# Optimization experiments

Hardware: AMD Instinct MI355X
Metric: run time of the kernel (lower is better)

Reference implementation:

```python
import jax, jax.numpy as jnp
import numpy as np


def setup_inputs() -> dict:
    key = jax.random.key(0)
    ks = jax.random.split(key, 5)
    B, N, C = 64, 384, 768
    return {
        "x": jax.random.normal(ks[0], (B, N, C), dtype=jnp.float32),
        "x_hsi": jax.random.normal(ks[1], (B, N, C), dtype=jnp.float32),
        "qkv_w": jax.random.normal(ks[2], (3 * C, C), dtype=jnp.float32) * 0.02,
        "proj_w": jax.random.normal(ks[3], (C, C), dtype=jnp.float32) * 0.02,
        "proj_b": jax.random.normal(ks[4], (C,), dtype=jnp.float32) * 0.02,
        "t_h": 8,
        "t_w": 8,
        "s_h": 16,
        "s_w": 16,
        "num_heads": 12,
    }


def reference(x, x_hsi, qkv_w, proj_w, proj_b, t_h, t_w, s_h, s_w, num_heads):
    B, N, C = x.shape
    H = num_heads
    Dh = C // H
    scale = Dh ** -0.5
    Lt = t_h * t_w * 2  # template tokens (2 templates)

    def qkv_heads(inp):
        qkv = (inp @ qkv_w.T).reshape(B, N, 3, H, Dh)
        qkv = jnp.transpose(qkv, (2, 0, 3, 1, 4))  # [3,B,H,N,Dh]
        return qkv[0], qkv[1], qkv[2]

    q, k, v = qkv_heads(x)
    q_hsi, k_hsi, v_hsi = qkv_heads(x_hsi)

    q_mt, q_s = q[:, :, :Lt], q[:, :, Lt:]
    k_mt, v_mt = k[:, :, :Lt], v[:, :, :Lt]
    q_s_hsi = q_hsi[:, :, Lt:]

    def attn(qq, kk, vv):
        a = jax.nn.softmax(jnp.einsum('bhqd,bhkd->bhqk', qq, kk) * scale, axis=-1)
        o = jnp.einsum('bhqk,bhkd->bhqd', a, vv)
        return jnp.transpose(o, (0, 2, 1, 3)).reshape(B, -1, C)

    x_mt = attn(q_mt, k_mt, v_mt)        # template-template
    x_s = attn(q_s, k, v)                # search attends to all
    x_s_hsi = attn(q_s_hsi, k_hsi, v_hsi)  # hsi search attends to all hsi

    out = jnp.concatenate([x_mt, x_s], axis=1) @ proj_w.T + proj_b
    out_hsi = jnp.concatenate([x_mt, x_s_hsi], axis=1) @ proj_w.T + proj_b
    return out, out_hsi
```

## Files before the change

kernel.cpp:

```cpp
#include <hip/hip_runtime.h>

typedef __attribute__((ext_vector_type(8))) short short8;
typedef __attribute__((ext_vector_type(4))) short bf16x4;
typedef __attribute__((ext_vector_type(4))) float f32x4;

__device__ __forceinline__ f32x4 mfma16(short8 a, short8 b, f32x4 c) {
  return __builtin_amdgcn_mfma_f32_16x16x32_bf16(a, b, c, 0, 0, 0);
}

__device__ __forceinline__ short f2bf(float f) {
  union { float f; unsigned u; } v; v.f = f;
  unsigned r = (v.u + 0x7fffu + ((v.u >> 16) & 1u)) >> 16;
  return (short)r;
}

__device__ __forceinline__ void gload16(const short* g, short* l) {
  __builtin_amdgcn_global_load_lds(
      (const __attribute__((address_space(1))) void*)g,
      (__attribute__((address_space(3))) void*)l, 16, 0, 0);
}

__global__ __launch_bounds__(256) void cvt_k(const float* __restrict__ src,
                                             short* __restrict__ dst, long n8) {
  long i = (long)blockIdx.x * 256 + threadIdx.x;
  const long stride = (long)gridDim.x * 256;
  for (; i < n8; i += stride) {
    float4 a = *(const float4*)(src + i * 8);
    float4 b = *(const float4*)(src + i * 8 + 4);
    short8 o = {f2bf(a.x), f2bf(a.y), f2bf(a.z), f2bf(a.w),
                f2bf(b.x), f2bf(b.y), f2bf(b.z), f2bf(b.w)};
    *(short8*)(dst + i * 8) = o;
  }
}

__device__ __forceinline__ void gemm256_core(
    const short* a00, const short* a01, const short* a10, const short* a11,
    const short* b00, const short* b01, const short* b10, const short* b11,
    char* lds, int wv, int lane, f32x4 (&acc)[8][4]) {
  const int l15 = lane & 15, q4 = lane >> 4;
  const int wm = wv & 1, wn = wv >> 1;
  const char* rdA = lds + wm * 16384;
  const char* rdB = lds + 32768 + (wn >> 1) * 16384;
  const int rB0 = (wn & 1) * 64;

  auto stg = [&](int T, int h, int tt) {
    const int t = tt >= 12 ? tt - 12 : tt;
    char* d = lds + (t & 1) * 65536 + T * 32768 + h * 16384 + wv * 2048;
    const short* g0 = T ? (h ? b10 : b00) : (h ? a10 : a00);
    const short* g1 = T ? (h ? b11 : b01) : (h ? a11 : a01);
    gload16(g0 + t * 64, (short*)d);
    gload16(g1 + t * 64, (short*)(d + 1024));
  };
  auto rdfrag = [&](const char* base, int rowl, int ks) -> short8 {
    int off = ks * 8192 + rowl * 64 + q4 * 16;
    off ^= ((off >> 9) & 1) << 5;
    return *(const short8*)(base + off);
  };

  stg(0, 0, 0); stg(0, 1, 0); stg(1, 0, 0); stg(1, 1, 0);
  stg(1, 0, 1); stg(1, 1, 1);
  asm volatile("s_waitcnt vmcnt(4)" ::: "memory");
  __builtin_amdgcn_s_barrier();

  auto ktile = [&](int buf, int t) {
    const char* A = rdA + buf * 65536;
    const char* B = rdB + buf * 65536;
    short8 af[4][2], bfr[4][2];
#pragma unroll
    for (int m = 0; m < 4; ++m) {
      af[m][0] = rdfrag(A, m * 16 + l15, 0);
      af[m][1] = rdfrag(A, m * 16 + l15, 1);
    }
#pragma unroll
    for (int n = 0; n < 2; ++n) {
      bfr[n][0] = rdfrag(B, rB0 + n * 16 + l15, 0);
      bfr[n][1] = rdfrag(B, rB0 + n * 16 + l15, 1);
    }
    stg(0, 0, t + 1);
    __builtin_amdgcn_s_barrier();
    __builtin_amdgcn_s_setprio(1);
#pragma unroll
    for (int m = 0; m < 4; ++m)
#pragma unroll
      for (int n = 0; n < 2; ++n) {
        acc[m][n] = mfma16(af[m][0], bfr[n][0], acc[m][n]);
        acc[m][n] = mfma16(af[m][1], bfr[n][1], acc[m][n]);
      }
    __builtin_amdgcn_s_setprio(0);
    __builtin_amdgcn_s_barrier();
#pragma unroll
    for (int n = 2; n < 4; ++n) {
      bfr[n][0] = rdfrag(B, rB0 + n * 16 + l15, 0);
      bfr[n][1] = rdfrag(B, rB0 + n * 16 + l15, 1);
    }
    stg(0, 1, t + 1);
    __builtin_amdgcn_s_barrier();
    __builtin_amdgcn_s_setprio(1);
#pragma unroll
    for (int m = 0; m < 4; ++m)
#pragma unroll
      for (int n = 2; n < 4; ++n) {
        acc[m][n] = mfma16(af[m][0], bfr[n][0], acc[m][n]);
        acc[m][n] = mfma16(af[m][1], bfr[n][1], acc[m][n]);
      }
    __builtin_amdgcn_s_setprio(0);
    __builtin_amdgcn_s_barrier();
#pragma unroll
    for (int m = 0; m < 4; ++m) {
      af[m][0] = rdfrag(A, (m + 4) * 16 + l15, 0);
      af[m][1] = rdfrag(A, (m + 4) * 16 + l15, 1);
    }
    stg(1, 0, t + 2);
    __builtin_amdgcn_s_barrier();
    __builtin_amdgcn_s_setprio(1);
#pragma unroll
    for (int m = 0; m < 4; ++m)
#pragma unroll
      for (int n = 0; n < 2; ++n) {
        acc[m + 4][n] = mfma16(af[m][0], bfr[n][0], acc[m + 4][n]);
        acc[m + 4][n] = mfma16(af[m][1], bfr[n][1], acc[m + 4][n]);
      }
    __builtin_amdgcn_s_setprio(0);
    __builtin_amdgcn_s_barrier();
    stg(1, 1, t + 2);
    __builtin_amdgcn_s_barrier();
    __builtin_amdgcn_s_setprio(1);
#pragma unroll
    for (int m = 0; m < 4; ++m)
#pragma unroll
      for (int n = 2; n < 4; ++n) {
        acc[m + 4][n] = mfma16(af[m][0], bfr[n][0], acc[m + 4][n]);
        acc[m + 4][n] = mfma16(af[m][1], bfr[n][1], acc[m + 4][n]);
      }
    __builtin_amdgcn_s_setprio(0);
    asm volatile("s_waitcnt vmcnt(4)" ::: "memory");
    __builtin_amdgcn_s_barrier();
  };

  for (int g = 0; g < 6; ++g) {
    ktile(0, 2 * g);
    ktile(1, 2 * g + 1);
  }
}

__device__ __forceinline__ void stage_geom(int wv, int lane, int* srow, int* coff) {
#pragma unroll
  for (int j = 0; j < 2; ++j) {
    const int s = wv * 128 + j * 64 + lane;
    srow[j] = (s >> 2) & 127;
    coff[j] = (s >> 9) * 32 + (((((s & 3) << 4) ^ (((s >> 5) & 1) << 5))) >> 1);
  }
}

__global__ __launch_bounds__(512, 2) void gemm_qkv_k(
    const short* __restrict__ A0, const short* __restrict__ A1,
    const short* __restrict__ W,
    short* __restrict__ O0, short* __restrict__ O1) {
  extern __shared__ char lds[];
  const int tid = threadIdx.x, lane = tid & 63, wv = tid >> 6;
  const int l15 = lane & 15, q4 = lane >> 4;
  const int m0 = blockIdx.x * 256, n0 = blockIdx.y * 256;
  const short* A = blockIdx.z ? A1 : A0;
  short* O = blockIdx.z ? O1 : O0;

  int srow[2], coff[2];
  stage_geom(wv, lane, srow, coff);
  const short* a00 = A + (long)(m0 + srow[0]) * 768 + coff[0];
  const short* a01 = A + (long)(m0 + srow[1]) * 768 + coff[1];
  const short* a10 = A + (long)(m0 + 128 + srow[0]) * 768 + coff[0];
  const short* a11 = A + (long)(m0 + 128 + srow[1]) * 768 + coff[1];
  const short* b00 = W + (long)(n0 + srow[0]) * 768 + coff[0];
  const short* b01 = W + (long)(n0 + srow[1]) * 768 + coff[1];
  const short* b10 = W + (long)(n0 + 128 + srow[0]) * 768 + coff[0];
  const short* b11 = W + (long)(n0 + 128 + srow[1]) * 768 + coff[1];

  f32x4 acc[8][4] = {};
  gemm256_core(a00, a01, a10, a11, b00, b01, b10, b11, lds, wv, lane, acc);

  const int wm = wv & 1, wn = wv >> 1;
#pragma unroll
  for (int m = 0; m < 8; ++m)
#pragma unroll
    for (int n = 0; n < 4; ++n) {
      const int col = n0 + wn * 64 + n * 16 + l15;
#pragma unroll
      for (int r = 0; r < 4; ++r) {
        const int row = m0 + wm * 128 + m * 16 + q4 * 4 + r;
        O[(long)row * 2304 + col] = f2bf(acc[m][n][r]);
      }
    }
}

template <int NK>
__global__ __launch_bounds__(256) void attn_k(
    const short* __restrict__ qkvx, const short* __restrict__ qkvh,
    short* __restrict__ omt, short* __restrict__ os, short* __restrict__ osh) {
  constexpr int NT = NK / 16;
  constexpr int KT = NK / 64;
  constexpr int T = (NK == 128) ? 2 : 8;
  __shared__ __align__(16) short kv[2][64 * 72];
  __shared__ __align__(16) short sp[2][4][16 * 72];

  const int tid = threadIdx.x, lane = tid & 63, wv = tid >> 6;
  const int l15 = lane & 15, q4 = lane >> 4;
  const int bx = blockIdx.x;
  const int b = bx / (12 * T);
  const int rr = bx % (12 * T);
  const int h = rr / T, t = rr % T;

  const short* src;
  short* outb;
  int q0;
  if (NK == 128) {
    src = qkvx;
    outb = omt + ((long)b * 128 + t * 64) * 768 + h * 64;
    q0 = t * 64;
  } else {
    const int tt = t & 3;
    const bool hs = t >= 4;
    src = hs ? qkvh : qkvx;
    outb = (hs ? osh : os) + ((long)b * 256 + tt * 64) * 768 + h * 64;
    q0 = 128 + tt * 64;
  }
  const short* qb = src + ((long)(b * 384 + q0 + wv * 16)) * 2304 + h * 64;
  const short* kb = src + (long)b * 384 * 2304 + 768 + h * 64;
  const short* vb = kb + 768;

  const int key0 = tid >> 3, dg0 = tid & 7;
  const int key1 = key0 + 32, dg1 = dg0;

  short8 qf0 = *(const short8*)(qb + (long)l15 * 2304 + q4 * 8);
  short8 qf1 = *(const short8*)(qb + (long)l15 * 2304 + 32 + q4 * 8);

  f32x4 sacc[NT] = {};
  short8 ka0 = *(const short8*)(kb + (long)key0 * 2304 + dg0 * 8);
  short8 ka1 = *(const short8*)(kb + (long)key1 * 2304 + dg1 * 8);
#pragma unroll
  for (int kt = 0; kt < KT; ++kt) {
    const int buf = kt & 1;
    *(short8*)&kv[buf][key0 * 72 + dg0 * 8] = ka0;
    *(short8*)&kv[buf][key1 * 72 + dg1 * 8] = ka1;
    __syncthreads();
    if (kt + 1 < KT) {
      ka0 = *(const short8*)(kb + (long)((kt + 1) * 64 + key0) * 2304 + dg0 * 8);
      ka1 = *(const short8*)(kb + (long)((kt + 1) * 64 + key1) * 2304 + dg1 * 8);
    }
#pragma unroll
    for (int j = 0; j < 4; ++j) {
      short8 kf0 = *(const short8*)&kv[buf][(j * 16 + l15) * 72 + q4 * 8];
      short8 kf1 = *(const short8*)&kv[buf][(j * 16 + l15) * 72 + 32 + q4 * 8];
      sacc[kt * 4 + j] = mfma16(qf0, kf0, sacc[kt * 4 + j]);
      sacc[kt * 4 + j] = mfma16(qf1, kf1, sacc[kt * 4 + j]);
    }
  }

  short8 va0 = *(const short8*)(vb + (long)key0 * 2304 + dg0 * 8);
  short8 va1 = *(const short8*)(vb + (long)key1 * 2304 + dg1 * 8);

  const float scale = 0.125f;
  float mx[4] = {-3e38f, -3e38f, -3e38f, -3e38f};
#pragma unroll
  for (int nt = 0; nt < NT; ++nt)
#pragma unroll
    for (int r = 0; r < 4; ++r) mx[r] = fmaxf(mx[r], sacc[nt][r]);
#pragma unroll
  for (int r = 0; r < 4; ++r) {
    mx[r] = fmaxf(mx[r], __shfl_xor(mx[r], 1));
    mx[r] = fmaxf(mx[r], __shfl_xor(mx[r], 2));
    mx[r] = fmaxf(mx[r], __shfl_xor(mx[r], 4));
    mx[r] = fmaxf(mx[r], __shfl_xor(mx[r], 8));
  }
  float sm[4] = {0.f, 0.f, 0.f, 0.f};
  unsigned pb[NT][2];
#pragma unroll
  for (int nt = 0; nt < NT; ++nt) {
    float ev[4];
#pragma unroll
    for (int r = 0; r < 4; ++r) {
      ev[r] = __expf((sacc[nt][r] - mx[r]) * scale);
      sm[r] += ev[r];
    }
    pb[nt][0] = (unsigned)(unsigned short)f2bf(ev[0]) |
                ((unsigned)(unsigned short)f2bf(ev[1]) << 16);
    pb[nt][1] = (unsigned)(unsigned short)f2bf(ev[2]) |
                ((unsigned)(unsigned short)f2bf(ev[3]) << 16);
  }
#pragma unroll
  for (int r = 0; r < 4; ++r) {
    sm[r] += __shfl_xor(sm[r], 1);
    sm[r] += __shfl_xor(sm[r], 2);
    sm[r] += __shfl_xor(sm[r], 4);
    sm[r] += __shfl_xor(sm[r], 8);
  }

  f32x4 oacc[4] = {};
#pragma unroll
  for (int kt = 0; kt < KT; ++kt) {
    const int buf = kt & 1;
    char* vt = (char*)&kv[buf][0];
#pragma unroll
    for (int e = 0; e < 8; ++e) {
      const int d0 = dg0 * 8 + e;
      *(short*)(vt + ((d0 * 144 + key0 * 2) ^ (dg0 << 4))) = va0[e];
      *(short*)(vt + ((d0 * 144 + key1 * 2) ^ (dg1 << 4))) = va1[e];
    }
    short* spw = &sp[buf][wv][0];
#pragma unroll
    for (int nt2 = 0; nt2 < 4; ++nt2) {
#pragma unroll
      for (int p = 0; p < 2; ++p) {
        const unsigned w = pb[kt * 4 + nt2][p];
        spw[(q4 * 4 + 2 * p) * 72 + nt2 * 16 + l15] = (short)(w & 0xffffu);
        spw[(q4 * 4 + 2 * p + 1) * 72 + nt2 * 16 + l15] = (short)(w >> 16);
      }
    }
    __syncthreads();
    if (kt + 1 < KT) {
      va0 = *(const short8*)(vb + (long)((kt + 1) * 64 + key0) * 2304 + dg0 * 8);
      va1 = *(const short8*)(vb + (long)((kt + 1) * 64 + key1) * 2304 + dg1 * 8);
    }
#pragma unroll
    for (int ks = 0; ks < 2; ++ks) {
      short8 pf = *(const short8*)&sp[buf][wv][l15 * 72 + ks * 32 + q4 * 8];
#pragma unroll
      for (int n2 = 0; n2 < 4; ++n2) {
        const int db = n2 * 16 + l15;
        short8 vf = *(const short8*)(vt + ((db * 144 + (ks * 32 + q4 * 8) * 2) ^
                                           (((db >> 3) & 7) << 4)));
        oacc[n2] = mfma16(pf, vf, oacc[n2]);
      }
    }
  }

  short* ob = outb + wv * 16 * 768;
#pragma unroll
  for (int r = 0; r < 4; ++r) {
    const float inv = 1.f / sm[r];
#pragma unroll
    for (int n2 = 0; n2 < 4; ++n2)
      ob[(q4 * 4 + r) * 768 + n2 * 16 + l15] = f2bf(oacc[n2][r] * inv);
  }
}

__global__ __launch_bounds__(512, 2) void gemm_proj_k(
    const short* __restrict__ mt, const short* __restrict__ sA,
    const short* __restrict__ sh,
    const short* __restrict__ W, const float* __restrict__ bias,
    float* __restrict__ out, int cb0) {
  extern __shared__ char lds[];
  const int tid = threadIdx.x, lane = tid & 63, wv = tid >> 6;
  const int l15 = lane & 15, q4 = lane >> 4;
  const int m0 = blockIdx.x * 256, n0 = blockIdx.y * 256;
  const short* s = blockIdx.z ? sh : sA;

  int srow[2], coff[2];
  stage_geom(wv, lane, srow, coff);
  auto arow = [&](int r) -> const short* {
    const int ba = r / 384, na = r % 384;
    return na < 128 ? (mt + ((long)ba * 128 + na) * 768)
                    : (s + ((long)ba * 256 + (na - 128)) * 768);
  };
  const short* a00 = arow(m0 + srow[0]) + coff[0];
  const short* a01 = arow(m0 + srow[1]) + coff[1];
  const short* a10 = arow(m0 + 128 + srow[0]) + coff[0];
  const short* a11 = arow(m0 + 128 + srow[1]) + coff[1];
  const short* b00 = W + (long)(n0 + srow[0]) * 768 + coff[0];
  const short* b01 = W + (long)(n0 + srow[1]) * 768 + coff[1];
  const short* b10 = W + (long)(n0 + 128 + srow[0]) * 768 + coff[0];
  const short* b11 = W + (long)(n0 + 128 + srow[1]) * 768 + coff[1];

  f32x4 acc[8][4] = {};
  gemm256_core(a00, a01, a10, a11, b00, b01, b10, b11, lds, wv, lane, acc);

  const int wm = wv & 1, wn = wv >> 1;
#pragma unroll
  for (int n = 0; n < 4; ++n) {
    const int col = n0 + wn * 64 + n * 16 + l15;
    const float bvv = bias[col];
#pragma unroll
    for (int m = 0; m < 8; ++m)
#pragma unroll
      for (int r = 0; r < 4; ++r) {
        const int row = m0 + wm * 128 + m * 16 + q4 * 4 + r;
        out[(long)blockIdx.z * 18874368 + ((long)cb0 * 384 + row) * 768 + col] =
            acc[m][n][r] + bvv;
      }
  }
}

extern "C" void kernel_launch(void* const* d_in, const int* in_sizes, int n_in,
                              void* d_out, int out_size, void* d_ws, size_t ws_size,
                              hipStream_t stream) {
  (void)in_sizes; (void)n_in; (void)out_size;
  const float* x  = (const float*)d_in[0];
  const float* xh = (const float*)d_in[1];
  const float* qw = (const float*)d_in[2];
  const float* pw = (const float*)d_in[3];
  const float* pb = (const float*)d_in[4];
  float* out = (float*)d_out;

  const long qwSz = 2304L * 768 * 2;
  const long pwSz = 768L * 768 * 2;
  const long fixedW = qwSz + pwSz;
  const long perBatch = (2L * 384 * 768 + 2L * 384 * 2304 + 640L * 768) * 2;
  int CB = 64;
  while (CB > 2 && (long)CB * perBatch + fixedW > (long)ws_size) CB >>= 1;

  char* ws = (char*)d_ws;
  short* qwbf = (short*)ws;
  short* pwbf = (short*)(ws + qwSz);
  char* dyn = ws + fixedW;
  const long xbfSz = (long)CB * 384 * 768 * 2;
  const long qkvSz = (long)CB * 384 * 2304 * 2;
  const long mtSz  = (long)CB * 128 * 768 * 2;
  const long sSz   = (long)CB * 256 * 768 * 2;
  short* xbf  = (short*)dyn;
  short* xhbf = (short*)(dyn + xbfSz);
  short* qkvx = (short*)(dyn + 2 * xbfSz);
  short* qkvh = (short*)(dyn + 2 * xbfSz + qkvSz);
  short* amt  = (short*)(dyn + 2 * xbfSz + 2 * qkvSz);
  short* as_  = (short*)(dyn + 2 * xbfSz + 2 * qkvSz + mtSz);
  short* ash  = (short*)(dyn + 2 * xbfSz + 2 * qkvSz + mtSz + sSz);

  cvt_k<<<864, 256, 0, stream>>>(qw, qwbf, 2304L * 768 / 8);
  cvt_k<<<288, 256, 0, stream>>>(pw, pwbf, 768L * 768 / 8);

  const int nch = 64 / CB;
  for (int c = 0; c < nch; ++c) {
    const int cb0 = c * CB;
    const long n8 = (long)CB * 384 * 768 / 8;
    cvt_k<<<2048, 256, 0, stream>>>(x + (long)cb0 * 384 * 768, xbf, n8);
    cvt_k<<<2048, 256, 0, stream>>>(xh + (long)cb0 * 384 * 768, xhbf, n8);
    dim3 g1((CB * 384) / 256, 9, 2);
    gemm_qkv_k<<<g1, 512, 131072, stream>>>(xbf, xhbf, qwbf, qkvx, qkvh);
    attn_k<128><<<CB * 12 * 2, 256, 0, stream>>>(qkvx, qkvh, amt, as_, ash);
    attn_k<384><<<CB * 12 * 8, 256, 0, stream>>>(qkvx, qkvh, amt, as_, ash);
    dim3 g3((CB * 384) / 256, 3, 2);
    gemm_proj_k<<<g3, 512, 131072, stream>>>(amt, as_, ash, pwbf, pb, out, cb0);
  }
}
```

Measured before the change: 712.1 us.

## Rewrite attention as flash-style online softmax with multi-row query tiles per wave

Attention now uses online-softmax rescaling. Each wave handles several 16-row query blocks (32 or 64 rows), so every block covers all queries of one batch-head and each K/V tile loaded into LDS is reused across more queries. K and V are staged together in a single pass over the keys, removing the second pass and the large per-row score register array. The QKV GEMM inner step is also reordered to load fragments per k-slice across all four N tiles. Costs are fewer blocks per launch, which may reduce occupancy, and more registers per wave.

After: 872.0 us. 22.5% more time.

```diff
diff --git a/kernel.cpp b/kernel.cpp
--- a/kernel.cpp
+++ b/kernel.cpp
@@ -65,73 +65,57 @@
   auto ktile = [&](int buf, int t) {
     const char* A = rdA + buf * 65536;
     const char* B = rdB + buf * 65536;
-    short8 af[4][2], bfr[4][2];
-#pragma unroll
-    for (int m = 0; m < 4; ++m) {
-      af[m][0] = rdfrag(A, m * 16 + l15, 0);
-      af[m][1] = rdfrag(A, m * 16 + l15, 1);
-    }
-#pragma unroll
-    for (int n = 0; n < 2; ++n) {
-      bfr[n][0] = rdfrag(B, rB0 + n * 16 + l15, 0);
-      bfr[n][1] = rdfrag(B, rB0 + n * 16 + l15, 1);
-    }
+    short8 afl[4], bfr[4][2];
+#pragma unroll
+    for (int m = 0; m < 4; ++m) afl[m] = rdfrag(A, m * 16 + l15, 0);
+#pragma unroll
+    for (int n = 0; n < 4; ++n) bfr[n][0] = rdfrag(B, rB0 + n * 16 + l15, 0);
     stg(0, 0, t + 1);
     __builtin_amdgcn_s_barrier();
     __builtin_amdgcn_s_setprio(1);
 #pragma unroll
     for (int m = 0; m < 4; ++m)
 #pragma unroll
-      for (int n = 0; n < 2; ++n) {
-        acc[m][n] = mfma16(af[m][0], bfr[n][0], acc[m][n]);
-        acc[m][n] = mfma16(af[m][1], bfr[n][1], acc[m][n]);
-      }
+      for (int n = 0; n < 4; ++n)
+        acc[m][n] = mfma16(afl[m], bfr[n][0], acc[m][n]);
     __builtin_amdgcn_s_setprio(0);
     __builtin_amdgcn_s_barrier();
 #pragma unroll
-    for (int n = 2; n < 4; ++n) {
-      bfr[n][0] = rdfrag(B, rB0 + n * 16 + l15, 0);
-      bfr[n][1] = rdfrag(B, rB0 + n * 16 + l15, 1);
-    }
+    for (int m = 0; m < 4; ++m) afl[m] = rdfrag(A, m * 16 + l15, 1);
+#pragma unroll
+    for (int n = 0; n < 4; ++n) bfr[n][1] = rdfrag(B, rB0 + n * 16 + l15, 1);
     stg(0, 1, t + 1);
     __builtin_amdgcn_s_barrier();
     __builtin_amdgcn_s_setprio(1);
 #pragma unroll
     for (int m = 0; m < 4; ++m)
 #pragma unroll
-      for (int n = 2; n < 4; ++n) {
-        acc[m][n] = mfma16(af[m][0], bfr[n][0], acc[m][n]);
-        acc[m][n] = mfma16(af[m][1], bfr[n][1], acc[m][n]);
-      }
+      for (int n = 0; n < 4; ++n)
+        acc[m][n] = mfma16(afl[m], bfr[n][1], acc[m][n]);
     __builtin_amdgcn_s_setprio(0);
     __builtin_amdgcn_s_barrier();
 #pragma unroll
-    for (int m = 0; m < 4; ++m) {
-      af[m][0] = rdfrag(A, (m + 4) * 16 + l15, 0);
-      af[m][1] = rdfrag(A, (m + 4) * 16 + l15, 1);
-    }
+    for (int m = 0; m < 4; ++m) afl[m] = rdfrag(A, (m + 4) * 16 + l15, 0);
     stg(1, 0, t + 2);
     __builtin_amdgcn_s_barrier();
     __builtin_amdgcn_s_setprio(1);
 #pragma unroll
     for (int m = 0; m < 4; ++m)
 #pragma unroll
-      for (int n = 0; n < 2; ++n) {
-        acc[m + 4][n] = mfma16(af[m][0], bfr[n][0], acc[m + 4][n]);
-        acc[m + 4][n] = mfma16(af[m][1], bfr[n][1], acc[m + 4][n]);
-      }
+      for (int n = 0; n < 4; ++n)
+        acc[m + 4][n] = mfma16(afl[m], bfr[n][0], acc[m + 4][n]);
     __builtin_amdgcn_s_setprio(0);
     __builtin_amdgcn_s_barrier();
+#pragma unroll
+    for (int m = 0; m < 4; ++m) afl[m] = rdfrag(A, (m + 4) * 16 + l15, 1);
     stg(1, 1, t + 2);
     __builtin_amdgcn_s_barrier();
     __builtin_amdgcn_s_setprio(1);
 #pragma unroll
     for (int m = 0; m < 4; ++m)
 #pragma unroll
-      for (int n = 2; n < 4; ++n) {
-        acc[m + 4][n] = mfma16(af[m][0], bfr[n][0], acc[m + 4][n]);
-        acc[m + 4][n] = mfma16(af[m][1], bfr[n][1], acc[m + 4][n]);
-      }
+      for (int n = 0; n < 4; ++n)
+        acc[m + 4][n] = mfma16(afl[m], bfr[n][1], acc[m + 4][n]);
     __builtin_amdgcn_s_setprio(0);
     asm volatile("s_waitcnt vmcnt(4)" ::: "memory");
     __builtin_amdgcn_s_barrier();
@@ -191,155 +175,161 @@
     }
 }
 
-template <int NK>
-__global__ __launch_bounds__(256) void attn_k(
+template <int NK, int QW>
+__global__ __launch_bounds__(256, 2) void attn_f(
     const short* __restrict__ qkvx, const short* __restrict__ qkvh,
     short* __restrict__ omt, short* __restrict__ os, short* __restrict__ osh) {
-  constexpr int NT = NK / 16;
   constexpr int KT = NK / 64;
-  constexpr int T = (NK == 128) ? 2 : 8;
-  __shared__ __align__(16) short kv[2][64 * 72];
-  __shared__ __align__(16) short sp[2][4][16 * 72];
+  constexpr int MB = QW / 16;
+  __shared__ __align__(16) short kk[2][64 * 72];
+  __shared__ __align__(16) short vvs[2][64 * 72];
+  __shared__ __align__(16) short sp[4][QW * 72];
 
   const int tid = threadIdx.x, lane = tid & 63, wv = tid >> 6;
   const int l15 = lane & 15, q4 = lane >> 4;
-  const int bx = blockIdx.x;
-  const int b = bx / (12 * T);
-  const int rr = bx % (12 * T);
-  const int h = rr / T, t = rr % T;
-
-  const short* src;
+  const int b = blockIdx.x, h = blockIdx.y, kind = blockIdx.z;
+
+  const short* src = kind ? qkvh : qkvx;
   short* outb;
   int q0;
   if (NK == 128) {
-    src = qkvx;
-    outb = omt + ((long)b * 128 + t * 64) * 768 + h * 64;
-    q0 = t * 64;
+    outb = omt + ((long)b * 128) * 768 + h * 64;
+    q0 = 0;
   } else {
-    const int tt = t & 3;
-    const bool hs = t >= 4;
-    src = hs ? qkvh : qkvx;
-    outb = (hs ? osh : os) + ((long)b * 256 + tt * 64) * 768 + h * 64;
-    q0 = 128 + tt * 64;
-  }
-  const short* qb = src + ((long)(b * 384 + q0 + wv * 16)) * 2304 + h * 64;
+    outb = (kind ? osh : os) + ((long)b * 256) * 768 + h * 64;
+    q0 = 128;
+  }
+  const short* qb = src + ((long)(b * 384 + q0 + wv * QW)) * 2304 + h * 64;
   const short* kb = src + (long)b * 384 * 2304 + 768 + h * 64;
   const short* vb = kb + 768;
 
   const int key0 = tid >> 3, dg0 = tid & 7;
-  const int key1 = key0 + 32, dg1 = dg0;
-
-  short8 qf0 = *(const short8*)(qb + (long)l15 * 2304 + q4 * 8);
-  short8 qf1 = *(const short8*)(qb + (long)l15 * 2304 + 32 + q4 * 8);
-
-  f32x4 sacc[NT] = {};
+  const int key1 = key0 + 32;
+
+  short8 qf[MB][2];
+#pragma unroll
+  for (int m = 0; m < MB; ++m)
+#pragma unroll
+    for (int ks = 0; ks < 2; ++ks)
+      qf[m][ks] = *(const short8*)(qb + (long)(m * 16 + l15) * 2304 + ks * 32 + q4 * 8);
+
+  float mxr[MB][4], smr[MB][4];
+  f32x4 oacc[MB][4] = {};
+#pragma unroll
+  for (int m = 0; m < MB; ++m)
+#pragma unroll
+    for (int r = 0; r < 4; ++r) { mxr[m][r] = -3e30f; smr[m][r] = 0.f; }
+
   short8 ka0 = *(const short8*)(kb + (long)key0 * 2304 + dg0 * 8);
-  short8 ka1 = *(const short8*)(kb + (long)key1 * 2304 + dg1 * 8);
-#pragma unroll
+  short8 ka1 = *(const short8*)(kb + (long)key1 * 2304 + dg0 * 8);
+  short8 va0 = *(const short8*)(vb + (long)key0 * 2304 + dg0 * 8);
+  short8 va1 = *(const short8*)(vb + (long)key1 * 2304 + dg0 * 8);
+
+  const float scale = 0.125f;
+  char* spw = (char*)&sp[wv][0];
+
   for (int kt = 0; kt < KT; ++kt) {
     const int buf = kt & 1;
-    *(short8*)&kv[buf][key0 * 72 + dg0 * 8] = ka0;
-    *(short8*)&kv[buf][key1 * 72 + dg1 * 8] = ka1;
+    *(short8*)&kk[buf][key0 * 72 + dg0 * 8] = ka0;
+    *(short8*)&kk[buf][key1 * 72 + dg0 * 8] = ka1;
+    char* vt = (char*)&vvs[buf][0];
+#pragma unroll
+    for (int e = 0; e < 8; ++e) {
+      const int d0 = dg0 * 8 + e;
+      *(short*)(vt + ((d0 * 144 + key0 * 2) ^ (dg0 << 4))) = va0[e];
+      *(short*)(vt + ((d0 * 144 + key1 * 2) ^ (dg0 << 4))) = va1[e];
+    }
     __syncthreads();
     if (kt + 1 < KT) {
       ka0 = *(const short8*)(kb + (long)((kt + 1) * 64 + key0) * 2304 + dg0 * 8);
-      ka1 = *(const short8*)(kb + (long)((kt + 1) * 64 + key1) * 2304 + dg1 * 8);
-    }
-#pragma unroll
-    for (int j = 0; j < 4; ++j) {
-      short8 kf0 = *(const short8*)&kv[buf][(j * 16 + l15) * 72 + q4 * 8];
-      short8 kf1 = *(const short8*)&kv[buf][(j * 16 + l15) * 72 + 32 + q4 * 8];
-      sacc[kt * 4 + j] = mfma16(qf0, kf0, sacc[kt * 4 + j]);
-      sacc[kt * 4 + j] = mfma16(qf1, kf1, sacc[kt * 4 + j]);
-    }
-  }
-
-  short8 va0 = *(const short8*)(vb + (long)key0 * 2304 + dg0 * 8);
-  short8 va1 = *(const short8*)(vb + (long)key1 * 2304 + dg1 * 8);
-
-  const float scale = 0.125f;
-  float mx[4] = {-3e38f, -3e38f, -3e38f, -3e38f};
-#pragma unroll
-  for (int nt = 0; nt < NT; ++nt)
-#pragma unroll
-    for (int r = 0; r < 4; ++r) mx[r] = fmaxf(mx[r], sacc[nt][r]);
-#pragma unroll
-  for (int r = 0; r < 4; ++r) {
-    mx[r] = fmaxf(mx[r], __shfl_xor(mx[r], 1));
-    mx[r] = fmaxf(mx[r], __shfl_xor(mx[r], 2));
-    mx[r] = fmaxf(mx[r], __shfl_xor(mx[r], 4));
-    mx[r] = fmaxf(mx[r], __shfl_xor(mx[r], 8));
-  }
-  float sm[4] = {0.f, 0.f, 0.f, 0.f};
-  unsigned pb[NT][2];
-#pragma unroll
-  for (int nt = 0; nt < NT; ++nt) {
-    float ev[4];
-#pragma unroll
-    for (int r = 0; r < 4; ++r) {
-      ev[r] = __expf((sacc[nt][r] - mx[r]) * scale);
-      sm[r] += ev[r];
-    }
-    pb[nt][0] = (unsigned)(unsigned short)f2bf(ev[0]) |
-                ((unsigned)(unsigned short)f2bf(ev[1]) << 16);
-    pb[nt][1] = (unsigned)(unsigned short)f2bf(ev[2]) |
-                ((unsigned)(unsigned short)f2bf(ev[3]) << 16);
-  }
-#pragma unroll
-  for (int r = 0; r < 4; ++r) {
-    sm[r] += __shfl_xor(sm[r], 1);
-    sm[r] += __shfl_xor(sm[r], 2);
-    sm[r] += __shfl_xor(sm[r], 4);
-    sm[r] += __shfl_xor(sm[r], 8);
-  }
-
-  f32x4 oacc[4] = {};
-#pragma unroll
-  for (int kt = 0; kt < KT; ++kt) {
-    const int buf = kt & 1;
-    char* vt = (char*)&kv[buf][0];
-#pragma unroll
-    for (int e = 0; e < 8; ++e) {
-      const int d0 = dg0 * 8 + e;
-      *(short*)(vt + ((d0 * 144 + key0 * 2) ^ (dg0 << 4))) = va0[e];
-      *(short*)(vt + ((d0 * 144 + key1 * 2) ^ (dg1 << 4))) = va1[e];
-    }
-    short* spw = &sp[buf][wv][0];
-#pragma unroll
-    for (int nt2 = 0; nt2 < 4; ++nt2) {
-#pragma unroll
-      for (int p = 0; p < 2; ++p) {
-        const unsigned w = pb[kt * 4 + nt2][p];
-        spw[(q4 * 4 + 2 * p) * 72 + nt2 * 16 + l15] = (short)(w & 0xffffu);
-        spw[(q4 * 4 + 2 * p + 1) * 72 + nt2 * 16 + l15] = (short)(w >> 16);
-      }
-    }
-    __syncthreads();
-    if (kt + 1 < KT) {
+      ka1 = *(const short8*)(kb + (long)((kt + 1) * 64 + key1) * 2304 + dg0 * 8);
       va0 = *(const short8*)(vb + (long)((kt + 1) * 64 + key0) * 2304 + dg0 * 8);
-      va1 = *(const short8*)(vb + (long)((kt + 1) * 64 + key1) * 2304 + dg1 * 8);
-    }
+      va1 = *(const short8*)(vb + (long)((kt + 1) * 64 + key1) * 2304 + dg0 * 8);
+    }
+
+    f32x4 sacc[MB][4] = {};
+#pragma unroll
+    for (int n = 0; n < 4; ++n) {
+      short8 kf0 = *(const short8*)&kk[buf][(n * 16 + l15) * 72 + q4 * 8];
+      short8 kf1 = *(const short8*)&kk[buf][(n * 16 + l15) * 72 + 32 + q4 * 8];
+#pragma unroll
+      for (int m = 0; m < MB; ++m) {
+        sacc[m][n] = mfma16(qf[m][0], kf0, sacc[m][n]);
+        sacc[m][n] = mfma16(qf[m][1], kf1, sacc[m][n]);
+      }
+    }
+
+#pragma unroll
+    for (int m = 0; m < MB; ++m) {
+      float pm[4];
+#pragma unroll
+      for (int r = 0; r < 4; ++r)
+        pm[r] = fmaxf(fmaxf(sacc[m][0][r], sacc[m][1][r]),
+                      fmaxf(sacc[m][2][r], sacc[m][3][r]));
+#pragma unroll
+      for (int r = 0; r < 4; ++r) {
+        pm[r] = fmaxf(pm[r], __shfl_xor(pm[r], 1));
+        pm[r] = fmaxf(pm[r], __shfl_xor(pm[r], 2));
+        pm[r] = fmaxf(pm[r], __shfl_xor(pm[r], 4));
+        pm[r] = fmaxf(pm[r], __shfl_xor(pm[r], 8));
+      }
+#pragma unroll
+      for (int r = 0; r < 4; ++r) {
+        const float mnew = fmaxf(mxr[m][r], pm[r]);
+        const float resc = __expf((mxr[m][r] - mnew) * scale);
+        mxr[m][r] = mnew;
+        smr[m][r] *= resc;
+#pragma unroll
+        for (int n2 = 0; n2 < 4; ++n2) oacc[m][n2][r] *= resc;
+      }
+#pragma unroll
+      for (int n = 0; n < 4; ++n)
+#pragma unroll
+        for (int r = 0; r < 4; ++r) {
+          const float e = __expf((sacc[m][n][r] - mxr[m][r]) * scale);
+          smr[m][r] += e;
+          const int row = m * 16 + q4 * 4 + r;
+          const int byte = (row * 144 + (n * 16 + l15) * 2) ^ (((row >> 3) & 1) << 5);
+          *(short*)(spw + byte) = f2bf(e);
+        }
+    }
+
 #pragma unroll
     for (int ks = 0; ks < 2; ++ks) {
-      short8 pf = *(const short8*)&sp[buf][wv][l15 * 72 + ks * 32 + q4 * 8];
+      short8 pf[MB];
+#pragma unroll
+      for (int m = 0; m < MB; ++m) {
+        const int row = m * 16 + l15;
+        const int byte = (row * 144 + ks * 64 + q4 * 16) ^ (((row >> 3) & 1) << 5);
+        pf[m] = *(const short8*)(spw + byte);
+      }
 #pragma unroll
       for (int n2 = 0; n2 < 4; ++n2) {
         const int db = n2 * 16 + l15;
         short8 vf = *(const short8*)(vt + ((db * 144 + (ks * 32 + q4 * 8) * 2) ^
                                            (((db >> 3) & 7) << 4)));
-        oacc[n2] = mfma16(pf, vf, oacc[n2]);
-      }
-    }
-  }
-
-  short* ob = outb + wv * 16 * 768;
-#pragma unroll
-  for (int r = 0; r < 4; ++r) {
-    const float inv = 1.f / sm[r];
-#pragma unroll
-    for (int n2 = 0; n2 < 4; ++n2)
-      ob[(q4 * 4 + r) * 768 + n2 * 16 + l15] = f2bf(oacc[n2][r] * inv);
-  }
+#pragma unroll
+        for (int m = 0; m < MB; ++m)
+          oacc[m][n2] = mfma16(pf[m], vf, oacc[m][n2]);
+      }
+    }
+  }
+
+  short* ob = outb + (long)wv * QW * 768;
+#pragma unroll
+  for (int m = 0; m < MB; ++m)
+#pragma unroll
+    for (int r = 0; r < 4; ++r) {
+      float s = smr[m][r];
+      s += __shfl_xor(s, 1);
+      s += __shfl_xor(s, 2);
+      s += __shfl_xor(s, 4);
+      s += __shfl_xor(s, 8);
+      const float inv = 1.f / s;
+#pragma unroll
+      for (int n2 = 0; n2 < 4; ++n2)
+        ob[(m * 16 + q4 * 4 + r) * 768 + n2 * 16 + l15] = f2bf(oacc[m][n2][r] * inv);
+    }
 }
 
 __global__ __launch_bounds__(512, 2) void gemm_proj_k(
@@ -433,8 +423,8 @@
     cvt_k<<<2048, 256, 0, stream>>>(xh + (long)cb0 * 384 * 768, xhbf, n8);
     dim3 g1((CB * 384) / 256, 9, 2);
     gemm_qkv_k<<<g1, 512, 131072, stream>>>(xbf, xhbf, qwbf, qkvx, qkvh);
-    attn_k<128><<<CB * 12 * 2, 256, 0, stream>>>(qkvx, qkvh, amt, as_, ash);
-    attn_k<384><<<CB * 12 * 8, 256, 0, stream>>>(qkvx, qkvh, amt, as_, ash);
+    attn_f<128, 32><<<dim3(CB, 12, 1), 256, 0, stream>>>(qkvx, qkvh, amt, as_, ash);
+    attn_f<384, 64><<<dim3(CB, 12, 2), 256, 0, stream>>>(qkvx, qkvh, amt, as_, ash);
     dim3 g3((CB * 384) / 256, 3, 2);
     gemm_proj_k<<<g3, 512, 131072, stream>>>(amt, as_, ash, pwbf, pb, out, cb0);
   }
```
